# Performance work log

Measured on AMD Instinct MI355X. Metric: run time of the kernel, lower is better.

The kernel has to match this reference:

```python
import jax, jax.numpy as jnp
import numpy as np

C = 2048      # in_dim (fixed by Incidence_matrix conv)
P = 8         # patch_size
HW = 64       # feature_size
BN_EPS = 1e-5


def setup_inputs() -> dict:
    key = jax.random.key(0)
    ks = jax.random.split(key, 12)
    B = 4
    x = jax.random.normal(ks[0], (B, C, HW, HW), dtype=jnp.float32)
    s = 0.02
    Wk = jax.random.normal(ks[1], (C // 8, C), dtype=jnp.float32) * s
    bk = jax.random.normal(ks[2], (C // 8,), dtype=jnp.float32) * s
    Wq = jax.random.normal(ks[3], (C // 8, C), dtype=jnp.float32) * s
    bq = jax.random.normal(ks[4], (C // 8,), dtype=jnp.float32) * s
    Wv = jax.random.normal(ks[5], (C, C), dtype=jnp.float32) * s
    bv = jax.random.normal(ks[6], (C,), dtype=jnp.float32) * s
    inc_W = jax.random.normal(ks[7], (256, C), dtype=jnp.float32) * s
    inc_b = jax.random.normal(ks[8], (256,), dtype=jnp.float32) * s
    bn_gamma = jnp.ones((256,), dtype=jnp.float32)
    bn_beta = jnp.zeros((256,), dtype=jnp.float32)
    bn_mean = jax.random.normal(ks[9], (256,), dtype=jnp.float32) * 0.1
    bn_var = jax.random.uniform(ks[10], (256,), dtype=jnp.float32) + 0.5
    return {"x": x, "Wk": Wk, "bk": bk, "Wq": Wq, "bq": bq, "Wv": Wv,
            "bv": bv, "inc_W": inc_W, "inc_b": inc_b, "bn_gamma": bn_gamma,
            "bn_beta": bn_beta, "bn_mean": bn_mean, "bn_var": bn_var}


def _forward(x, Wk, bk, Wq, bq, Wv, bv, inc_W, inc_b, bn_gamma, bn_beta, bn_mean, bn_var):
    B, Cc, H, W = x.shape
    nh, nw = H // P, W // P
    N = nh * nw
    Ck = Cc // 8

    # Incidence branch: 1x1 conv -> BN (eval) -> ReLU
    inc = jnp.einsum('bchw,kc->bkhw', x, inc_W) + inc_b[:, None, None]
    inc = (inc - bn_mean[:, None, None]) * (bn_gamma[:, None, None]
          / jnp.sqrt(bn_var[:, None, None] + BN_EPS)) + bn_beta[:, None, None]
    inc = jax.nn.relu(inc)
    # 4x4 avg/max pool (stride 4), then relu each and add
    inc5 = inc.reshape(B, 256, H // 4, 4, W // 4, 4)
    inc_pool = jax.nn.relu(inc5.mean((3, 5))) + jax.nn.relu(inc5.max((3, 5)))
    inc_flat = inc_pool.reshape(B, 256, -1)[:, :, :N]          # [B,256,N] (only first N cols used)

    # Patchify exactly as torch: rearrange 'b c (h p1)(w p2) -> b (h w)(p1 p2 c)'
    # then each flat (p1 p2 c) vector is reinterpreted (view) as (C,p,p).
    patches = (x.reshape(B, Cc, nh, P, nw, P)
                 .transpose(0, 2, 4, 3, 5, 1)                  # [B,nh,nw,p,p,C]
                 .reshape(B, N, Cc, P, P))                      # faithful scrambled view

    # Shared 1x1 KQV projections over all patches
    K = jnp.einsum('bncpq,kc->bnkpq', patches, Wk) + bk[:, None, None]   # [B,N,C/8,p,p]
    Q = jnp.einsum('bncpq,kc->bnkpq', patches, Wq) + bq[:, None, None]
    V = jnp.einsum('bncpq,kc->bnkpq', patches, Wv) + bv[:, None, None]   # [B,N,C,p,p]

    # Q_block = sum_i Q_i * incidence scalar per channel
    Q_block = jnp.einsum('bnkpq,bkn->bkpq', Q, inc_flat)        # [B,C/8,p,p]

    Jp = Q_block.reshape(B, Ck, P * P).transpose(0, 2, 1)        # [B,p2,C/8]
    Kp = K.reshape(B, N, Ck, P * P)                              # [B,N,C/8,p2]
    scores = jnp.einsum('bxc,bncy->bnxy', Jp, Kp)                # [B,N,p2,p2]
    A = jax.nn.softmax(scores, axis=2)                           # torch softmax dim=1
    Vp = V.reshape(B, N, Cc, P * P)                              # [B,N,C,p2]
    out = jnp.einsum('bncx,bnxy->bncy', Vp, A)                   # [B,N,C,p2]

    # cat along height then view back to [B,C,H,W] (faithful scrambled reshape)
    out = out.transpose(0, 2, 1, 3).reshape(B, Cc, H, W)
    return out + x


def reference(x, Wk, bk, Wq, bq, Wv, bv, inc_W, inc_b, bn_gamma, bn_beta, bn_mean, bn_var):
    return _forward(x, Wk, bk, Wq, bq, Wv, bv, inc_W, inc_b,
                    bn_gamma, bn_beta, bn_mean, bn_var)
```

## Files before the change

kernel.cpp:

```cpp
#include <hip/hip_runtime.h>
#include <cstdint>
#include <cstddef>


typedef _Float16 f16_t;
typedef __attribute__((ext_vector_type(8))) _Float16 f16x8;
typedef __attribute__((ext_vector_type(4))) _Float16 f16x4;
typedef __attribute__((ext_vector_type(4))) float f32x4;

#define GLD16(gsrc, ldst) __builtin_amdgcn_global_load_lds( \
    (__attribute__((address_space(1))) void*)(gsrc),        \
    (__attribute__((address_space(3))) void*)(ldst), 16, 0, 0)

#define SBAR() do { __builtin_amdgcn_sched_barrier(0); \
                    __builtin_amdgcn_s_barrier();      \
                    __builtin_amdgcn_sched_barrier(0); } while (0)

#define LGKM0() do { asm volatile("s_waitcnt lgkmcnt(0)" ::: "memory"); \
                     __builtin_amdgcn_sched_barrier(0); } while (0)

template<int N> __device__ __forceinline__ void wvm() {
  if constexpr (N == 0)       asm volatile("s_waitcnt vmcnt(0)" ::: "memory");
  else if constexpr (N == 2)  asm volatile("s_waitcnt vmcnt(2)" ::: "memory");
  else if constexpr (N == 4)  asm volatile("s_waitcnt vmcnt(4)" ::: "memory");
  else if constexpr (N == 6)  asm volatile("s_waitcnt vmcnt(6)" ::: "memory");
  else if constexpr (N == 8)  asm volatile("s_waitcnt vmcnt(8)" ::: "memory");
  __builtin_amdgcn_sched_barrier(0);
}

__device__ __forceinline__ void split16(float v, f16_t& h, f16_t& l) {
  h = (f16_t)v;
  l = (f16_t)(v - (float)h);
}

__global__ __launch_bounds__(256)
void prep_kernel(const float* __restrict__ Wk, const float* __restrict__ bk,
                 const float* __restrict__ Wq, const float* __restrict__ bq,
                 const float* __restrict__ Wv, const float* __restrict__ incW,
                 f16_t* __restrict__ Wkq_a0, f16_t* __restrict__ Wkq_a1,
                 f16_t* __restrict__ Wv_f,
                 f16_t* __restrict__ incW_a0, f16_t* __restrict__ incW_a1,
                 float* __restrict__ bias_kq)
{
  __shared__ float lds[2048];
  const int row = blockIdx.x;
  const int t = threadIdx.x;
  const float* src;
  f16_t* d0;
  f16_t* d1;
  bool permute = true;
  if (row < 256) {
    src = Wk + (size_t)row * 2048; d0 = Wkq_a0 + (size_t)row * 2048; d1 = Wkq_a1 + (size_t)row * 2048;
  } else if (row < 512) {
    src = Wq + (size_t)(row - 256) * 2048; d0 = Wkq_a0 + (size_t)row * 2048; d1 = Wkq_a1 + (size_t)row * 2048;
  } else if (row < 2560) {
    src = Wv + (size_t)(row - 512) * 2048; d0 = Wv_f + (size_t)(row - 512) * 2048; d1 = nullptr;
  } else {
    src = incW + (size_t)(row - 2560) * 2048; d0 = incW_a0 + (size_t)(row - 2560) * 2048;
    d1 = incW_a1 + (size_t)(row - 2560) * 2048; permute = false;
  }
#pragma unroll
  for (int i = 0; i < 8; ++i) lds[i * 256 + t] = src[i * 256 + t];
  if (row < 512 && t == 0) bias_kq[row] = (row < 256) ? bk[row] : bq[row - 256];
  __syncthreads();
#pragma unroll
  for (int i = 0; i < 8; ++i) {
    int kh = i * 256 + t;
    int cp = permute ? (((kh >> 3) & 7) * 256 + (kh & 7) * 32 + (kh >> 6)) : kh;
    float v = lds[cp];
    f16_t hh, ll;
    split16(v, hh, ll);
    d0[kh] = hh;
    if (d1) d1[kh] = ll;
  }
}

__global__ __launch_bounds__(256)
void gather_kernel(const float* __restrict__ x,
                   f16_t* __restrict__ P0, f16_t* __restrict__ P1)
{
  const int bid = blockIdx.x;
  const int b = bid >> 7;
  const int ph = (bid >> 4) & 7;
  const int cc = bid & 15;
  const int t = threadIdx.x;
  const int pix = t & 127;
  const int p1 = pix >> 4, p2q = pix & 15;
  const int w = p2q * 4;
  const int pw = w >> 3, p2 = w & 7;
  const size_t patch = (size_t)(b * 64 + ph * 8 + pw);
  for (int it = 0; it < 64; ++it) {
    int cl = it * 2 + (t >> 7);
    int c = cc * 128 + cl;
    int j = c & 63, tq = c >> 6;
    const float4 v = *(const float4*)&x[(((size_t)b * 2048 + c) * 64 + ph * 8 + p1) * 64 + w];
    size_t dst = patch * 131072 + (size_t)j * 2048 + tq * 64 + p1 * 8 + p2;
    float vv[4] = {v.x, v.y, v.z, v.w};
    f16x4 h, l;
#pragma unroll
    for (int u = 0; u < 4; ++u) {
      f16_t hh, ll;
      split16(vv[u], hh, ll);
      h[u] = hh; l[u] = ll;
    }
    *(f16x4*)&P0[dst] = h;
    *(f16x4*)&P1[dst] = l;
  }
}

__global__ __launch_bounds__(256)
void xt_kernel(const float* __restrict__ x,
               f16_t* __restrict__ T0, f16_t* __restrict__ T1)
{
  __shared__ float lds[64][65];
  const int bid = blockIdx.x;
  const int b = bid >> 9;
  const int h = (bid >> 5) & 15;
  const int cc = bid & 31;
  const int t = threadIdx.x;
  {
    int ci = t >> 2, w4 = t & 3;
    const float* src = &x[(((size_t)b * 2048 + cc * 64 + ci) * 64 + h) * 64];
#pragma unroll
    for (int it = 0; it < 4; ++it) {
      int w0 = it * 16 + w4 * 4;
      const float4 v = *(const float4*)&src[w0];
      lds[ci][w0 + 0] = v.x; lds[ci][w0 + 1] = v.y;
      lds[ci][w0 + 2] = v.z; lds[ci][w0 + 3] = v.w;
    }
  }
  __syncthreads();
  const int w = t >> 2, cq = t & 3;
  const size_t rowbase = ((size_t)b * 1024 + h * 64 + w) * 2048 + cc * 64 + cq * 16;
  f16x8 H0, H1, L0, L1;
#pragma unroll
  for (int u = 0; u < 8; ++u) {
    f16_t hh, ll;
    split16(lds[cq * 16 + u][w], hh, ll);
    H0[u] = hh; L0[u] = ll;
  }
#pragma unroll
  for (int u = 0; u < 8; ++u) {
    f16_t hh, ll;
    split16(lds[cq * 16 + 8 + u][w], hh, ll);
    H1[u] = hh; L1[u] = ll;
  }
  *(f16x8*)&T0[rowbase] = H0; *(f16x8*)&T0[rowbase + 8] = H1;
  *(f16x8*)&T1[rowbase] = L0; *(f16x8*)&T1[rowbase + 8] = L1;
}

template<int PHASES, int EPI, int SLICES>
__global__ __launch_bounds__(256)
void gemm_kernel(const f16_t* __restrict__ A0, const f16_t* __restrict__ A1,
                 const f16_t* __restrict__ B0, const f16_t* __restrict__ B1,
                 float* __restrict__ Cf, f16_t* __restrict__ Cb,
                 const float* __restrict__ bias, int MB, int ldc)
{
  __shared__ f16_t As[128 * 64];
  __shared__ f16_t Bs[128 * 64];
  const int nwg = gridDim.x;
  const int q = nwg >> 3;
  const int bid = ((int)blockIdx.x & 7) * q + ((int)blockIdx.x >> 3);
  const int tiles = nwg / SLICES;
  const int slice = bid / tiles;
  const int rem = bid % tiles;
  const int nb = rem / MB, mb = rem % MB;
  const int m0 = mb * 128, n0 = nb * 128;
  const int t = threadIdx.x;
  const int lane = t & 63, wv = t >> 6;
  const int wm = (wv >> 1) * 64, wn = (wv & 1) * 64;
  const int l15 = lane & 15, l4 = lane >> 4;

  const f32x4 vzero = {0.f, 0.f, 0.f, 0.f};
  f32x4 acc[4][4];
#pragma unroll
  for (int i = 0; i < 4; ++i)
#pragma unroll
    for (int j = 0; j < 4; ++j) acc[i][j] = vzero;

  constexpr int LOCAL = (32 * PHASES) / SLICES;
  for (int s = 0; s < LOCAL; ++s) {
    const int step = slice * LOCAL + s;
    const int ph = step >> 5;
    const int k0 = (step & 31) << 6;
    const f16_t* Ab = (PHASES == 3 && ph == 2) ? A1 : A0;
    const f16_t* Bb = (PHASES == 3 && ph == 1) ? B1 : B0;
    __syncthreads();
#pragma unroll
    for (int i = 0; i < 4; ++i) {
      int e = i * 2048 + t * 8;
      int row = e >> 6;
      int gl = ((e >> 3) & 7) ^ (row & 7);
      GLD16(Ab + (size_t)(m0 + row) * 2048 + k0 + gl * 8, &As[e]);
    }
#pragma unroll
    for (int i = 0; i < 4; ++i) {
      int e = i * 2048 + t * 8;
      int row = e >> 6;
      int gl = ((e >> 3) & 7) ^ (row & 7);
      GLD16(Bb + (size_t)(n0 + row) * 2048 + k0 + gl * 8, &Bs[e]);
    }
    __syncthreads();
#pragma unroll
    for (int ks = 0; ks < 2; ++ks) {
      f16x8 a[4], bb[4];
#pragma unroll
      for (int i = 0; i < 4; ++i) {
        int r = wm + i * 16 + l15;
        int g = (ks * 4 + l4) ^ (r & 7);
        a[i] = *(const f16x8*)&As[r * 64 + g * 8];
      }
#pragma unroll
      for (int j = 0; j < 4; ++j) {
        int r = wn + j * 16 + l15;
        int g = (ks * 4 + l4) ^ (r & 7);
        bb[j] = *(const f16x8*)&Bs[r * 64 + g * 8];
      }
#pragma unroll
      for (int i = 0; i < 4; ++i)
#pragma unroll
        for (int j = 0; j < 4; ++j)
          acc[i][j] = __builtin_amdgcn_mfma_f32_16x16x32_f16(a[i], bb[j], acc[i][j], 0, 0, 0);
    }
  }

  float* Cp = (EPI == 0) ? Cf + (size_t)slice * (size_t)MB * 128 * (size_t)ldc : nullptr;
#pragma unroll
  for (int i = 0; i < 4; ++i) {
#pragma unroll
    for (int j = 0; j < 4; ++j) {
      int nloc = n0 + wn + j * 16 + l15;
#pragma unroll
      for (int r = 0; r < 4; ++r) {
        int m = m0 + wm + i * 16 + l4 * 4 + r;
        float bsv = (SLICES == 1 || slice == 0) ? bias[m] : 0.f;
        float v = acc[i][j][r] + bsv;
        if (EPI == 0) {
          Cp[(size_t)m * ldc + nloc] = v;
        } else {
          int patch = nloc >> 6, jj = nloc & 63;
          Cb[(size_t)patch * 131072 + (size_t)m * 64 + jj] = (f16_t)v;
        }
      }
    }
  }
}

#define RDA(dst, RH) \
  _Pragma("unroll") for (int i = 0; i < MIQ; ++i) \
  _Pragma("unroll") for (int ks = 0; ks < 2; ++ks) { \
    int r = wm * WTM + (RH) * (WTM / 2) + i * 16 + l15; \
    dst[i][ks] = *(const f16x8*)&lds[cb + r * 64 + (((ks * 4 + l4) ^ (r & 7)) << 3)]; \
  }
#define RDB(dst, CH) \
  _Pragma("unroll") for (int j = 0; j < NJQ; ++j) \
  _Pragma("unroll") for (int ks = 0; ks < 2; ++ks) { \
    int r = wn * WTN + (CH) * (WTN / 2) + j * 16 + l15; \
    dst[j][ks] = *(const f16x8*)&lds[cb + BBASE + r * 64 + (((ks * 4 + l4) ^ (r & 7)) << 3)]; \
  }
#define QMFMA(AR, BR, RH, CH) do { \
  __builtin_amdgcn_s_setprio(1); \
  _Pragma("unroll") for (int ks = 0; ks < 2; ++ks) \
  _Pragma("unroll") for (int i = 0; i < MIQ; ++i) \
  _Pragma("unroll") for (int j = 0; j < NJQ; ++j) \
    acc[(RH) * MIQ + i][(CH) * NJQ + j] = __builtin_amdgcn_mfma_f32_16x16x32_f16( \
        AR[i][ks], BR[j][ks], acc[(RH) * MIQ + i][(CH) * NJQ + j], 0, 0, 0); \
  __builtin_amdgcn_s_setprio(0); } while (0)

template<int NPH, int EPI, int BM, int BN, int WM, int WN, int MBT>
__global__ __launch_bounds__(512, 2)
void gemm8_kernel(const f16_t* __restrict__ A0f, const f16_t* __restrict__ A1f,
                  const f16_t* __restrict__ B0f, const f16_t* __restrict__ B1f,
                  float* __restrict__ Cf, f16_t* __restrict__ Cb,
                  const float* __restrict__ bias, int ldc)
{
  constexpr int WTM = BM / WM, WTN = BN / WN;
  constexpr int MIQ = WTM / 32, NJQ = WTN / 32;
  constexpr int GA = BM / 128, GB = BN / 128;
  constexpr int BBASE = BM * 64;
  constexpr int BUF = (BM + BN) * 64;
  constexpr int NT = 32 * NPH;
  constexpr int VW = 2 * GB;
  __shared__ f16_t lds[2 * BUF];

  const int nwg = gridDim.x;
  const int q = nwg >> 3;
  const int bid = ((int)blockIdx.x & 7) * q + ((int)blockIdx.x >> 3);
  const int mb = bid % MBT, nb = bid / MBT;
  const int m0 = mb * BM, n0 = nb * BN;
  const int tid = threadIdx.x;
  const int lane = tid & 63;
  const int wv = tid >> 6;
  const int wm = wv / WN, wn = wv % WN;
  const int l15 = lane & 15, l4 = lane >> 4;

  auto stageA = [&](int tt, int rg) {
    if (tt >= NT) return;
    const f16_t* s = (NPH == 3 && (tt >> 5) == 2) ? A1f : A0f;
    const int g0 = m0 + rg * (BM / 2);
    const int base = (tt & 1) * BUF + rg * (BM / 2) * 64;
    const int k0 = (tt & 31) << 6;
#pragma unroll
    for (int i = 0; i < GA; ++i) {
      int idx = i * 4096 + tid * 8;
      int r = idx >> 6, sl = (idx >> 3) & 7;
      GLD16(s + (size_t)(g0 + r) * 2048 + k0 + ((sl ^ (r & 7)) << 3), &lds[base + idx]);
    }
  };
  auto stageB = [&](int tt, int rg) {
    if (tt >= NT) return;
    const f16_t* s = (NPH == 3 && (tt >> 5) == 1) ? B1f : B0f;
    const int g0 = n0 + rg * (BN / 2);
    const int base = (tt & 1) * BUF + BBASE + rg * (BN / 2) * 64;
    const int k0 = (tt & 31) << 6;
#pragma unroll
    for (int i = 0; i < GB; ++i) {
      int idx = i * 4096 + tid * 8;
      int r = idx >> 6, sl = (idx >> 3) & 7;
      GLD16(s + (size_t)(g0 + r) * 2048 + k0 + ((sl ^ (r & 7)) << 3), &lds[base + idx]);
    }
  };

  const f32x4 vzero = {0.f, 0.f, 0.f, 0.f};
  f32x4 acc[WTM / 16][WTN / 16];
#pragma unroll
  for (int i = 0; i < WTM / 16; ++i)
#pragma unroll
    for (int j = 0; j < WTN / 16; ++j) acc[i][j] = vzero;

  stageA(0, 0); stageA(0, 1); stageB(0, 0); stageB(0, 1);
  stageB(1, 0); stageB(1, 1);
  wvm<VW>();
  SBAR();

  for (int tt = 0; tt < NT; ++tt) {
    const int cb = (tt & 1) * BUF;
    f16x8 a0[MIQ][2], a1[MIQ][2], b0[NJQ][2], b1[NJQ][2];
    RDA(a0, 0); RDB(b0, 0);
    stageA(tt + 1, 0);
    SBAR(); LGKM0();
    QMFMA(a0, b0, 0, 0);
    SBAR();
    RDB(b1, 1);
    stageA(tt + 1, 1);
    SBAR(); LGKM0();
    QMFMA(a0, b1, 0, 1);
    SBAR();
    RDA(a1, 1);
    stageB(tt + 2, 0);
    SBAR(); LGKM0();
    QMFMA(a1, b0, 1, 0);
    SBAR();
    stageB(tt + 2, 1);
    if (tt < NT - 2) { wvm<VW>(); } else { wvm<0>(); }
    SBAR();
    QMFMA(a1, b1, 1, 1);
    SBAR();
  }

#pragma unroll
  for (int i = 0; i < WTM / 16; ++i) {
#pragma unroll
    for (int j = 0; j < WTN / 16; ++j) {
      int ncol = n0 + wn * WTN + j * 16 + l15;
#pragma unroll
      for (int r = 0; r < 4; ++r) {
        int m = m0 + wm * WTM + i * 16 + l4 * 4 + r;
        float v = acc[i][j][r] + bias[m];
        if (EPI == 0) {
          Cf[(size_t)m * ldc + ncol] = v;
        } else {
          int patch = ncol >> 6, jj = ncol & 63;
          Cb[(size_t)patch * 131072 + (size_t)m * 64 + jj] = (f16_t)v;
        }
      }
    }
  }
}

__global__ void pool_kernel(const float* __restrict__ incout,
                            const float* __restrict__ bnmean, const float* __restrict__ bnvar,
                            const float* __restrict__ gamma, const float* __restrict__ beta,
                            float* __restrict__ incf)
{
  const int blk = blockIdx.x;
  const int b = blk >> 8, k = blk & 255;
  const int n = threadIdx.x;
  const int r = n >> 4, cq = n & 15;
  const float sc = gamma[k] * rsqrtf(bnvar[k] + 1e-5f);
  const float sh = beta[k] - bnmean[k] * sc;
  const size_t PSTR = (size_t)256 * 4096;
  const size_t base = (size_t)k * 4096 + b * 1024 + (r * 4) * 64 + cq * 4;
  float sum = 0.f, mx = 0.f;
#pragma unroll
  for (int dr = 0; dr < 4; ++dr)
#pragma unroll
    for (int dw = 0; dw < 4; ++dw) {
      size_t idx = base + dr * 64 + dw;
      float raw = incout[idx] + incout[idx + PSTR] + incout[idx + 2 * PSTR];
      float v = fmaxf(raw * sc + sh, 0.f);
      sum += v; mx = fmaxf(mx, v);
    }
  incf[(size_t)blk * 64 + n] = sum * (1.f / 16.f) + mx;
}

__global__ void qblock_kernel(const float* __restrict__ KQ,
                              const float* __restrict__ incf,
                              float* __restrict__ Qb)
{
  const int blk = blockIdx.x;
  const int b = blk >> 8, k = blk & 255;
  const int x = threadIdx.x;
  const float* qrow = KQ + (size_t)(256 + k) * 16384 + (size_t)b * 4096;
  const float* ivec = incf + (size_t)blk * 64;
  float a0 = 0.f, a1 = 0.f, a2 = 0.f, a3 = 0.f;
#pragma unroll
  for (int n = 0; n < 16; ++n) {
    a0 += qrow[n * 64 + x] * ivec[n];
    a1 += qrow[(n + 16) * 64 + x] * ivec[n + 16];
    a2 += qrow[(n + 32) * 64 + x] * ivec[n + 32];
    a3 += qrow[(n + 48) * 64 + x] * ivec[n + 48];
  }
  Qb[(size_t)blk * 64 + x] = (a0 + a1) + (a2 + a3);
}

__global__ __launch_bounds__(256)
void scores_kernel(const float* __restrict__ KQ, const float* __restrict__ Qb,
                   f16_t* __restrict__ Asm)
{
  __shared__ float Qs[64 * 64];
  __shared__ float Ks[64 * 64];
  const int pg = blockIdx.x;
  const int b = pg >> 6;
  const int t = threadIdx.x;
  const int y = t >> 2, xg = t & 3;
  float s[16];
#pragma unroll
  for (int i = 0; i < 16; ++i) s[i] = 0.f;
  for (int kc = 0; kc < 4; ++kc) {
    __syncthreads();
#pragma unroll
    for (int i = 0; i < 16; ++i) {
      int idx = i * 256 + t;
      Qs[idx] = Qb[(size_t)b * 16384 + kc * 4096 + idx];
      int kl = idx >> 6, yy = idx & 63;
      Ks[idx] = KQ[(size_t)(kc * 64 + kl) * 16384 + (size_t)pg * 64 + yy];
    }
    __syncthreads();
    float sc[16];
#pragma unroll
    for (int i = 0; i < 16; ++i) sc[i] = 0.f;
    for (int k = 0; k < 64; ++k) {
      float kv = Ks[k * 64 + y];
      const float4* qr = (const float4*)&Qs[k * 64 + xg * 16];
#pragma unroll
      for (int q4 = 0; q4 < 4; ++q4) {
        float4 qv = qr[q4];
        sc[q4 * 4 + 0] += qv.x * kv;
        sc[q4 * 4 + 1] += qv.y * kv;
        sc[q4 * 4 + 2] += qv.z * kv;
        sc[q4 * 4 + 3] += qv.w * kv;
      }
    }
#pragma unroll
    for (int i = 0; i < 16; ++i) s[i] += sc[i];
  }
  float mx = s[0];
#pragma unroll
  for (int i = 1; i < 16; ++i) mx = fmaxf(mx, s[i]);
  mx = fmaxf(mx, __shfl_xor(mx, 1));
  mx = fmaxf(mx, __shfl_xor(mx, 2));
  float p[16], sum = 0.f;
#pragma unroll
  for (int i = 0; i < 16; ++i) { p[i] = expf(s[i] - mx); sum += p[i]; }
  sum += __shfl_xor(sum, 1);
  sum += __shfl_xor(sum, 2);
  const float rinv = 1.f / sum;
#pragma unroll
  for (int i = 0; i < 16; ++i)
    Asm[(size_t)pg * 4096 + y * 64 + xg * 16 + i] = (f16_t)(p[i] * rinv);
}

__global__ __launch_bounds__(256)
void final_kernel(const f16_t* __restrict__ V, const f16_t* __restrict__ Asm,
                  const float* __restrict__ xin, float* __restrict__ out)
{
  __shared__ f16_t Vs[256 * 64];
  __shared__ f16_t Ps[64 * 64];
  const int bid = blockIdx.x;
  const int pg = bid >> 3, cb = bid & 7;
  const int b = pg >> 6, nl = pg & 63;
  const int t = threadIdx.x;
  const int lane = t & 63, wv = t >> 6;
  const int l15 = lane & 15, l4 = lane >> 4;
  const int wm = wv * 64;

#pragma unroll
  for (int i = 0; i < 8; ++i) {
    int e = i * 2048 + t * 8;
    int row = e >> 6;
    int gl = ((e >> 3) & 7) ^ (row & 7);
    GLD16(V + (size_t)pg * 131072 + (size_t)(cb * 256 + row) * 64 + gl * 8, &Vs[e]);
  }
#pragma unroll
  for (int i = 0; i < 2; ++i) {
    int e = i * 2048 + t * 8;
    int row = e >> 6;
    int gl = ((e >> 3) & 7) ^ (row & 7);
    GLD16(Asm + (size_t)pg * 4096 + (size_t)row * 64 + gl * 8, &Ps[e]);
  }
  __syncthreads();

  const f32x4 vzero = {0.f, 0.f, 0.f, 0.f};
  f32x4 acc[4][4];
#pragma unroll
  for (int i = 0; i < 4; ++i)
#pragma unroll
    for (int j = 0; j < 4; ++j) acc[i][j] = vzero;

#pragma unroll
  for (int ks = 0; ks < 2; ++ks) {
    f16x8 a[4], p[4];
#pragma unroll
    for (int i = 0; i < 4; ++i) {
      int r = wm + i * 16 + l15;
      int g = (ks * 4 + l4) ^ (r & 7);
      a[i] = *(const f16x8*)&Vs[r * 64 + g * 8];
    }
#pragma unroll
    for (int j = 0; j < 4; ++j) {
      int r = j * 16 + l15;
      int g = (ks * 4 + l4) ^ (r & 7);
      p[j] = *(const f16x8*)&Ps[r * 64 + g * 8];
    }
#pragma unroll
    for (int i = 0; i < 4; ++i)
#pragma unroll
      for (int j = 0; j < 4; ++j)
        acc[i][j] = __builtin_amdgcn_mfma_f32_16x16x32_f16(a[i], p[j], acc[i][j], 0, 0, 0);
  }

#pragma unroll
  for (int i = 0; i < 4; ++i) {
#pragma unroll
    for (int j = 0; j < 4; ++j) {
      int y = j * 16 + l15;
#pragma unroll
      for (int r = 0; r < 4; ++r) {
        int c = cb * 256 + wm + i * 16 + l4 * 4 + r;
        size_t idx = (((size_t)b * 2048 + c) * 64 + nl) * 64 + y;
        out[idx] = acc[i][j][r] + xin[idx];
      }
    }
  }
}

extern "C" void kernel_launch(void* const* d_in, const int* in_sizes, int n_in,
                              void* d_out, int out_size, void* d_ws, size_t ws_size,
                              hipStream_t stream) {
  const float* x     = (const float*)d_in[0];
  const float* Wk    = (const float*)d_in[1];
  const float* bk    = (const float*)d_in[2];
  const float* Wq    = (const float*)d_in[3];
  const float* bq    = (const float*)d_in[4];
  const float* Wv    = (const float*)d_in[5];
  const float* bv    = (const float*)d_in[6];
  const float* incW  = (const float*)d_in[7];
  const float* incb  = (const float*)d_in[8];
  const float* gamma = (const float*)d_in[9];
  const float* beta  = (const float*)d_in[10];
  const float* bnmean= (const float*)d_in[11];
  const float* bnvar = (const float*)d_in[12];

  char* ws = (char*)d_ws;
  f16_t* Wkq_a0 = (f16_t*)(ws + 0);
  f16_t* Wkq_a1 = (f16_t*)(ws + 2097152);
  f16_t* Wv_f   = (f16_t*)(ws + 4194304);
  f16_t* incW_a0= (f16_t*)(ws + 12582912);
  f16_t* incW_a1= (f16_t*)(ws + 13631488);
  float* biaskq = (float*) (ws + 14680064);
  float* incout = (float*) (ws + 14682112);
  float* incf   = (float*) (ws + 31459328);
  float* Qb     = (float*) (ws + 31721472);
  f16_t* Asm    = (f16_t*)(ws + 31983616);
  float* KQ     = (float*) (ws + 34080768);
  f16_t* xT_a0  = (f16_t*)(ws + 67635200);
  f16_t* xT_a1  = (f16_t*)(ws + 84412416);
  f16_t* P_a0   = (f16_t*)(ws + 101189632);
  f16_t* P_a1   = (f16_t*)(ws + 168298496);
  f16_t* Vbuf   = P_a1;

  prep_kernel<<<2816, 256, 0, stream>>>(Wk, bk, Wq, bq, Wv, incW,
                                        Wkq_a0, Wkq_a1, Wv_f, incW_a0, incW_a1, biaskq);
  gather_kernel<<<512, 256, 0, stream>>>(x, P_a0, P_a1);
  xt_kernel<<<2048, 256, 0, stream>>>(x, xT_a0, xT_a1);
  gemm_kernel<3, 0, 3><<<192, 256, 0, stream>>>(incW_a0, incW_a1, xT_a0, xT_a1,
                                                incout, nullptr, incb, 2, 4096);
  pool_kernel<<<1024, 64, 0, stream>>>(incout, bnmean, bnvar, gamma, beta, incf);
  gemm8_kernel<3, 0, 256, 128, 4, 2, 2><<<256, 512, 0, stream>>>(
      Wkq_a0, Wkq_a1, P_a0, P_a1, KQ, nullptr, biaskq, 16384);
  qblock_kernel<<<1024, 64, 0, stream>>>(KQ, incf, Qb);
  scores_kernel<<<256, 256, 0, stream>>>(KQ, Qb, Asm);
  gemm8_kernel<1, 1, 256, 256, 2, 4, 8><<<512, 512, 0, stream>>>(
      Wv_f, Wv_f, P_a0, P_a0, nullptr, Vbuf, bv, 64);
  final_kernel<<<2048, 256, 0, stream>>>(Vbuf, Asm, x, (float*)d_out);
}
```

Measured before the change: 487.0 us.

## Fuse V-projection GEMM with attention-apply and residual epilogue; tile patch gather through LDS

```diff
diff --git a/kernel.cpp b/kernel.cpp
--- a/kernel.cpp
+++ b/kernel.cpp
@@ -20,11 +20,11 @@
                      __builtin_amdgcn_sched_barrier(0); } while (0)
 
 template<int N> __device__ __forceinline__ void wvm() {
-  if constexpr (N == 0)       asm volatile("s_waitcnt vmcnt(0)" ::: "memory");
-  else if constexpr (N == 2)  asm volatile("s_waitcnt vmcnt(2)" ::: "memory");
-  else if constexpr (N == 4)  asm volatile("s_waitcnt vmcnt(4)" ::: "memory");
-  else if constexpr (N == 6)  asm volatile("s_waitcnt vmcnt(6)" ::: "memory");
-  else if constexpr (N == 8)  asm volatile("s_waitcnt vmcnt(8)" ::: "memory");
+  if constexpr (N == 0)      asm volatile("s_waitcnt vmcnt(0)" ::: "memory");
+  else if constexpr (N == 2) asm volatile("s_waitcnt vmcnt(2)" ::: "memory");
+  else if constexpr (N == 4) asm volatile("s_waitcnt vmcnt(4)" ::: "memory");
+  else if constexpr (N == 6) asm volatile("s_waitcnt vmcnt(6)" ::: "memory");
+  else if constexpr (N == 8) asm volatile("s_waitcnt vmcnt(8)" ::: "memory");
   __builtin_amdgcn_sched_barrier(0);
 }
 
@@ -79,32 +79,47 @@
 void gather_kernel(const float* __restrict__ x,
                    f16_t* __restrict__ P0, f16_t* __restrict__ P1)
 {
+  __shared__ float lds[16][8][68];
   const int bid = blockIdx.x;
-  const int b = bid >> 7;
-  const int ph = (bid >> 4) & 7;
-  const int cc = bid & 15;
+  const int b = bid >> 8;
+  const int ph = (bid >> 5) & 7;
+  const int tqc = (bid >> 2) & 7;
+  const int qq = bid & 3;
   const int t = threadIdx.x;
-  const int pix = t & 127;
-  const int p1 = pix >> 4, p2q = pix & 15;
-  const int w = p2q * 4;
-  const int pw = w >> 3, p2 = w & 7;
-  const size_t patch = (size_t)(b * 64 + ph * 8 + pw);
-  for (int it = 0; it < 64; ++it) {
-    int cl = it * 2 + (t >> 7);
-    int c = cc * 128 + cl;
-    int j = c & 63, tq = c >> 6;
-    const float4 v = *(const float4*)&x[(((size_t)b * 2048 + c) * 64 + ph * 8 + p1) * 64 + w];
-    size_t dst = patch * 131072 + (size_t)j * 2048 + tq * 64 + p1 * 8 + p2;
-    float vv[4] = {v.x, v.y, v.z, v.w};
-    f16x4 h, l;
-#pragma unroll
-    for (int u = 0; u < 4; ++u) {
-      f16_t hh, ll;
-      split16(vv[u], hh, ll);
-      h[u] = hh; l[u] = ll;
-    }
-    *(f16x4*)&P0[dst] = h;
-    *(f16x4*)&P1[dst] = l;
+  for (int k = 0; k < 4; ++k) {
+    const int chunk = qq * 4 + k;
+    const int cbase = tqc * 256 + chunk * 16;
+#pragma unroll
+    for (int it = 0; it < 8; ++it) {
+      int flat = it * 1024 + t * 4;
+      int ci = flat >> 9, p1 = (flat >> 6) & 7, w = flat & 63;
+      const float4 v = *(const float4*)&x[(((size_t)b * 2048 + cbase + ci) * 64 + ph * 8 + p1) * 64 + w];
+      *(float4*)&lds[ci][p1][w] = v;
+    }
+    __syncthreads();
+    const int tq = tqc * 4 + qq;
+    const int jb = k * 16;
+#pragma unroll
+    for (int it2 = 0; it2 < 8; ++it2) {
+      int flat2 = it2 * 256 + t;
+      int g = flat2 & 15, jp = flat2 >> 4;
+      int ji = jp >> 3, pw = jp & 7;
+      int p1 = g >> 1, w0 = pw * 8 + (g & 1) * 4;
+      const float4 v = *(const float4*)&lds[ji][p1][w0];
+      float vv[4] = {v.x, v.y, v.z, v.w};
+      f16x4 h, l;
+#pragma unroll
+      for (int u = 0; u < 4; ++u) {
+        f16_t hh, ll;
+        split16(vv[u], hh, ll);
+        h[u] = hh; l[u] = ll;
+      }
+      size_t pg = (size_t)(b * 64 + ph * 8 + pw);
+      size_t dst = pg * 131072 + (size_t)(jb + ji) * 2048 + tq * 64 + g * 4;
+      *(f16x4*)&P0[dst] = h;
+      *(f16x4*)&P1[dst] = l;
+    }
+    __syncthreads();
   }
 }
 
@@ -224,7 +239,7 @@
     }
   }
 
-  float* Cp = (EPI == 0) ? Cf + (size_t)slice * (size_t)MB * 128 * (size_t)ldc : nullptr;
+  float* Cp = Cf + (size_t)slice * (size_t)MB * 128 * (size_t)ldc;
 #pragma unroll
   for (int i = 0; i < 4; ++i) {
 #pragma unroll
@@ -234,13 +249,7 @@
       for (int r = 0; r < 4; ++r) {
         int m = m0 + wm + i * 16 + l4 * 4 + r;
         float bsv = (SLICES == 1 || slice == 0) ? bias[m] : 0.f;
-        float v = acc[i][j][r] + bsv;
-        if (EPI == 0) {
-          Cp[(size_t)m * ldc + nloc] = v;
-        } else {
-          int patch = nloc >> 6, jj = nloc & 63;
-          Cb[(size_t)patch * 131072 + (size_t)m * 64 + jj] = (f16_t)v;
-        }
+        Cp[(size_t)m * ldc + nloc] = acc[i][j][r] + bsv;
       }
     }
   }
@@ -271,8 +280,9 @@
 __global__ __launch_bounds__(512, 2)
 void gemm8_kernel(const f16_t* __restrict__ A0f, const f16_t* __restrict__ A1f,
                   const f16_t* __restrict__ B0f, const f16_t* __restrict__ B1f,
-                  float* __restrict__ Cf, f16_t* __restrict__ Cb,
-                  const float* __restrict__ bias, int ldc)
+                  float* __restrict__ Cf, const float* __restrict__ bias, int ldc,
+                  const f16_t* __restrict__ Amat, const float* __restrict__ Xin,
+                  float* __restrict__ Out)
 {
   constexpr int WTM = BM / WM, WTN = BN / WN;
   constexpr int MIQ = WTM / 32, NJQ = WTN / 32;
@@ -358,20 +368,67 @@
     SBAR();
   }
 
-#pragma unroll
-  for (int i = 0; i < WTM / 16; ++i) {
-#pragma unroll
-    for (int j = 0; j < WTN / 16; ++j) {
-      int ncol = n0 + wn * WTN + j * 16 + l15;
-#pragma unroll
-      for (int r = 0; r < 4; ++r) {
-        int m = m0 + wm * WTM + i * 16 + l4 * 4 + r;
-        float v = acc[i][j][r] + bias[m];
-        if (EPI == 0) {
-          Cf[(size_t)m * ldc + ncol] = v;
-        } else {
-          int patch = ncol >> 6, jj = ncol & 63;
-          Cb[(size_t)patch * 131072 + (size_t)m * 64 + jj] = (f16_t)v;
+  if constexpr (EPI == 2) {
+    f16_t* vl = &lds[wv * 8192];
+#pragma unroll
+    for (int i = 0; i < WTM / 16; ++i)
+#pragma unroll
+      for (int j = 0; j < WTN / 16; ++j)
+#pragma unroll
+        for (int r = 0; r < 4; ++r) {
+          int c = i * 16 + l4 * 4 + r;
+          int xx = j * 16 + l15;
+          float v = acc[i][j][r] + bias[m0 + wm * 128 + c];
+          vl[c * 64 + ((((xx >> 3) ^ (c & 7)) << 3) | (xx & 7))] = (f16_t)v;
+        }
+    const int pg = 4 * nb + wn;
+    f16x8 pb[4][2];
+#pragma unroll
+    for (int j = 0; j < 4; ++j)
+#pragma unroll
+      for (int ks = 0; ks < 2; ++ks)
+        pb[j][ks] = *(const f16x8*)&Amat[(size_t)pg * 4096 + (j * 16 + l15) * 64 + ks * 32 + l4 * 8];
+#pragma unroll
+    for (int i = 0; i < WTM / 16; ++i)
+#pragma unroll
+      for (int j = 0; j < WTN / 16; ++j) acc[i][j] = vzero;
+#pragma unroll
+    for (int i = 0; i < WTM / 16; ++i) {
+      f16x8 va[2];
+#pragma unroll
+      for (int ks = 0; ks < 2; ++ks) {
+        int c = i * 16 + l15;
+        va[ks] = *(const f16x8*)&vl[c * 64 + (((ks * 4 + l4) ^ (c & 7)) << 3)];
+      }
+#pragma unroll
+      for (int ks = 0; ks < 2; ++ks)
+#pragma unroll
+        for (int j = 0; j < 4; ++j)
+          acc[i][j] = __builtin_amdgcn_mfma_f32_16x16x32_f16(va[ks], pb[j][ks], acc[i][j], 0, 0, 0);
+    }
+    const int bb = pg >> 6, nl = pg & 63;
+    const size_t obase = ((size_t)bb * 2048 + m0 + wm * 128) * 4096 + (size_t)nl * 64;
+#pragma unroll
+    for (int i = 0; i < WTM / 16; ++i)
+#pragma unroll
+      for (int j = 0; j < 4; ++j)
+#pragma unroll
+        for (int r = 0; r < 4; ++r) {
+          int c = i * 16 + l4 * 4 + r;
+          int y = j * 16 + l15;
+          size_t idx = obase + (size_t)c * 4096 + y;
+          Out[idx] = acc[i][j][r] + Xin[idx];
+        }
+  } else {
+#pragma unroll
+    for (int i = 0; i < WTM / 16; ++i) {
+#pragma unroll
+      for (int j = 0; j < WTN / 16; ++j) {
+        int ncol = n0 + wn * WTN + j * 16 + l15;
+#pragma unroll
+        for (int r = 0; r < 4; ++r) {
+          int m = m0 + wm * WTM + i * 16 + l4 * 4 + r;
+          Cf[(size_t)m * ldc + ncol] = acc[i][j][r] + bias[m];
         }
       }
     }
@@ -479,80 +536,6 @@
 #pragma unroll
   for (int i = 0; i < 16; ++i)
     Asm[(size_t)pg * 4096 + y * 64 + xg * 16 + i] = (f16_t)(p[i] * rinv);
-}
-
-__global__ __launch_bounds__(256)
-void final_kernel(const f16_t* __restrict__ V, const f16_t* __restrict__ Asm,
-                  const float* __restrict__ xin, float* __restrict__ out)
-{
-  __shared__ f16_t Vs[256 * 64];
-  __shared__ f16_t Ps[64 * 64];
-  const int bid = blockIdx.x;
-  const int pg = bid >> 3, cb = bid & 7;
-  const int b = pg >> 6, nl = pg & 63;
-  const int t = threadIdx.x;
-  const int lane = t & 63, wv = t >> 6;
-  const int l15 = lane & 15, l4 = lane >> 4;
-  const int wm = wv * 64;
-
-#pragma unroll
-  for (int i = 0; i < 8; ++i) {
-    int e = i * 2048 + t * 8;
-    int row = e >> 6;
-    int gl = ((e >> 3) & 7) ^ (row & 7);
-    GLD16(V + (size_t)pg * 131072 + (size_t)(cb * 256 + row) * 64 + gl * 8, &Vs[e]);
-  }
-#pragma unroll
-  for (int i = 0; i < 2; ++i) {
-    int e = i * 2048 + t * 8;
-    int row = e >> 6;
-    int gl = ((e >> 3) & 7) ^ (row & 7);
-    GLD16(Asm + (size_t)pg * 4096 + (size_t)row * 64 + gl * 8, &Ps[e]);
-  }
-  __syncthreads();
-
-  const f32x4 vzero = {0.f, 0.f, 0.f, 0.f};
-  f32x4 acc[4][4];
-#pragma unroll
-  for (int i = 0; i < 4; ++i)
-#pragma unroll
-    for (int j = 0; j < 4; ++j) acc[i][j] = vzero;
-
-#pragma unroll
-  for (int ks = 0; ks < 2; ++ks) {
-    f16x8 a[4], p[4];
-#pragma unroll
-    for (int i = 0; i < 4; ++i) {
-      int r = wm + i * 16 + l15;
-      int g = (ks * 4 + l4) ^ (r & 7);
-      a[i] = *(const f16x8*)&Vs[r * 64 + g * 8];
-    }
-#pragma unroll
-    for (int j = 0; j < 4; ++j) {
-      int r = j * 16 + l15;
-      int g = (ks * 4 + l4) ^ (r & 7);
-      p[j] = *(const f16x8*)&Ps[r * 64 + g * 8];
-    }
-#pragma unroll
-    for (int i = 0; i < 4; ++i)
-#pragma unroll
-      for (int j = 0; j < 4; ++j)
-        acc[i][j] = __builtin_amdgcn_mfma_f32_16x16x32_f16(a[i], p[j], acc[i][j], 0, 0, 0);
-  }
-
-#pragma unroll
-  for (int i = 0; i < 4; ++i) {
-#pragma unroll
-    for (int j = 0; j < 4; ++j) {
-      int y = j * 16 + l15;
-#pragma unroll
-      for (int r = 0; r < 4; ++r) {
-        int c = cb * 256 + wm + i * 16 + l4 * 4 + r;
-        size_t idx = (((size_t)b * 2048 + c) * 64 + nl) * 64 + y;
-        out[idx] = acc[i][j][r] + xin[idx];
-      }
-    }
-  }
 }
 
 extern "C" void kernel_launch(void* const* d_in, const int* in_sizes, int n_in,
@@ -588,20 +571,18 @@
   f16_t* xT_a1  = (f16_t*)(ws + 84412416);
   f16_t* P_a0   = (f16_t*)(ws + 101189632);
   f16_t* P_a1   = (f16_t*)(ws + 168298496);
-  f16_t* Vbuf   = P_a1;
 
   prep_kernel<<<2816, 256, 0, stream>>>(Wk, bk, Wq, bq, Wv, incW,
                                         Wkq_a0, Wkq_a1, Wv_f, incW_a0, incW_a1, biaskq);
-  gather_kernel<<<512, 256, 0, stream>>>(x, P_a0, P_a1);
+  gather_kernel<<<1024, 256, 0, stream>>>(x, P_a0, P_a1);
   xt_kernel<<<2048, 256, 0, stream>>>(x, xT_a0, xT_a1);
   gemm_kernel<3, 0, 3><<<192, 256, 0, stream>>>(incW_a0, incW_a1, xT_a0, xT_a1,
                                                 incout, nullptr, incb, 2, 4096);
   pool_kernel<<<1024, 64, 0, stream>>>(incout, bnmean, bnvar, gamma, beta, incf);
   gemm8_kernel<3, 0, 256, 128, 4, 2, 2><<<256, 512, 0, stream>>>(
-      Wkq_a0, Wkq_a1, P_a0, P_a1, KQ, nullptr, biaskq, 16384);
+      Wkq_a0, Wkq_a1, P_a0, P_a1, KQ, biaskq, 16384, nullptr, nullptr, nullptr);
   qblock_kernel<<<1024, 64, 0, stream>>>(KQ, incf, Qb);
   scores_kernel<<<256, 256, 0, stream>>>(KQ, Qb, Asm);
-  gemm8_kernel<1, 1, 256, 256, 2, 4, 8><<<512, 512, 0, stream>>>(
-      Wv_f, Wv_f, P_a0, P_a0, nullptr, Vbuf, bv, 64);
-  final_kernel<<<2048, 256, 0, stream>>>(Vbuf, Asm, x, (float*)d_out);
-}
+  gemm8_kernel<1, 2, 256, 256, 2, 4, 8><<<512, 512, 0, stream>>>(
+      Wv_f, Wv_f, P_a0, P_a0, nullptr, bv, 0, Asm, x, (float*)d_out);
+}
```

Result: faster. 473.2 us (-2.8%).
